# Optimization experiments

Hardware: AMD Instinct MI355X
Metric: run time of the kernel (lower is better)

The kernel has to match this reference:

```python
import jax, jax.numpy as jnp
import numpy as np

NEG = -1e4      # BigBird additive mask value
LN_EPS = 1e-12  # BERT-style LayerNorm eps


def _bigbird_forward(xs_pad, mask, Wq, bq, Wk, bk, Wv, bv, Wo, bo, gamma, beta, rand_idx):
    b, n, hsz = xs_pad.shape
    H = rand_idx.shape[0]
    nb = rand_idx.shape[1] + 2          # one rand row per non-edge query block
    BS = n // nb                        # block size
    d = hsz // H
    r = rand_idx.shape[2]
    scale = 1.0 / np.sqrt(d).astype(np.float32)

    mf = mask.reshape(b, n).astype(xs_pad.dtype)   # (b,n) 1=token, 0=pad
    mb = mf.reshape(b, nb, BS)                     # blocked mask

    def proj(W, bias):
        return (xs_pad @ W + bias).reshape(b, n, H, d).transpose(0, 2, 1, 3)

    q = proj(Wq, bq) * scale            # (b,H,n,d)
    k = proj(Wk, bk)
    v = proj(Wv, bv)
    qb = q.reshape(b, H, nb, BS, d)
    kb = k.reshape(b, H, nb, BS, d)
    vb = v.reshape(b, H, nb, BS, d)

    # ---- global rows: first / last query block attend to all keys ----
    def full_row(qi):                   # qi: (b,H,BS,d)
        s = jnp.einsum('bhqd,bhkd->bhqk', qi, k) + (1.0 - mf)[:, None, None, :] * NEG
        return jnp.einsum('bhqk,bhkd->bhqd', jax.nn.softmax(s, axis=-1), v)

    ctx_first = full_row(qb[:, :, 0])
    ctx_last = full_row(qb[:, :, nb - 1])

    # ---- random key/value blocks: per-head, per-query-block gather ----
    hidx = jnp.arange(H)[:, None, None]
    rand_k = kb[:, hidx, rand_idx].reshape(b, H, nb - 2, r * BS, d)
    rand_v = vb[:, hidx, rand_idx].reshape(b, H, nb - 2, r * BS, d)
    rand_m = mb[:, rand_idx].reshape(b, H, nb - 2, r * BS)

    def sparse_row(qi, kc, vc, mc):     # kc:(b,H,K,d), mc:(b,H,K)
        s = jnp.einsum('bhqd,bhkd->bhqk', qi, kc) + (1.0 - mc)[:, :, None, :] * NEG
        return jnp.einsum('bhqk,bhkd->bhqd', jax.nn.softmax(s, axis=-1), vc)

    def gather_blocks(ids, ridx):
        kc = jnp.concatenate([kb[:, :, j] for j in ids] + [rand_k[:, :, ridx]], axis=2)
        vc = jnp.concatenate([vb[:, :, j] for j in ids] + [rand_v[:, :, ridx]], axis=2)
        mc = jnp.concatenate([jnp.broadcast_to(mb[:, None, j], (b, H, BS)) for j in ids]
                             + [rand_m[:, :, ridx]], axis=2)
        return kc, vc, mc

    # second / penultimate query blocks: window + globals + rand
    ctx_second = sparse_row(qb[:, :, 1], *gather_blocks([0, 1, 2, nb - 1], 0))
    ctx_penult = sparse_row(qb[:, :, nb - 2], *gather_blocks([nb - 3, nb - 2, nb - 1, 0], nb - 3))

    # ---- middle rows i in [2, nb-3]: 3-block sliding window + first/last global + r random ----
    nmid = nb - 4
    mid = jnp.arange(2, nb - 2)
    win = mid[:, None] + jnp.arange(-1, 2)[None, :]        # (nmid,3)
    k_win = kb[:, :, win].reshape(b, H, nmid, 3 * BS, d)
    v_win = vb[:, :, win].reshape(b, H, nmid, 3 * BS, d)
    m_win = jnp.broadcast_to(mb[:, win].reshape(b, 1, nmid, 3 * BS), (b, H, nmid, 3 * BS))

    def rep_glob(t):                     # (b,H,BS,...) -> (b,H,nmid,BS,...)
        return jnp.broadcast_to(t[:, :, None], (b, H, nmid) + t.shape[2:])

    k_mid = jnp.concatenate([k_win, rep_glob(kb[:, :, 0]), rep_glob(kb[:, :, nb - 1]),
                             rand_k[:, :, 1:nb - 3]], axis=3)
    v_mid = jnp.concatenate([v_win, rep_glob(vb[:, :, 0]), rep_glob(vb[:, :, nb - 1]),
                             rand_v[:, :, 1:nb - 3]], axis=3)
    m_first = jnp.broadcast_to(mb[:, None, None, 0], (b, H, nmid, BS))
    m_last = jnp.broadcast_to(mb[:, None, None, nb - 1], (b, H, nmid, BS))
    m_mid = jnp.concatenate([m_win, m_first, m_last, rand_m[:, :, 1:nb - 3]], axis=3)

    s_mid = jnp.einsum('bhmqd,bhmkd->bhmqk', qb[:, :, 2:nb - 2], k_mid) \
            + (1.0 - m_mid)[:, :, :, None, :] * NEG
    ctx_mid = jnp.einsum('bhmqk,bhmkd->bhmqd', jax.nn.softmax(s_mid, axis=-1), v_mid)

    ctx = jnp.concatenate([ctx_first[:, :, None], ctx_second[:, :, None], ctx_mid,
                           ctx_penult[:, :, None], ctx_last[:, :, None]], axis=2)
    ctx = ctx.reshape(b, H, n, d).transpose(0, 2, 1, 3).reshape(b, n, hsz)
    ctx = ctx * mf[:, :, None]           # from_mask on output rows

    # BigBirdSelfOutput: dense + residual + LayerNorm (dropout=0 / eval)
    y = ctx @ Wo + bo + xs_pad
    mu = y.mean(-1, keepdims=True)
    var = ((y - mu) ** 2).mean(-1, keepdims=True)
    return (y - mu) * jax.lax.rsqrt(var + LN_EPS) * gamma + beta


def setup_inputs() -> dict:
    key = jax.random.key(0)
    ks = jax.random.split(key, 6)
    B, N, HSZ, H, BS, R = 4, 4096, 1024, 16, 64, 3
    NB = N // BS
    init = lambda k, shp: jax.random.normal(k, shp, dtype=jnp.float32) * 0.02
    return {
        'xs_pad': jax.random.normal(ks[0], (B, N, HSZ), dtype=jnp.float32),
        'mask': jnp.ones((B, 1, N), dtype=jnp.int32),
        'Wq': init(ks[1], (HSZ, HSZ)), 'bq': jnp.zeros((HSZ,), jnp.float32),
        'Wk': init(ks[2], (HSZ, HSZ)), 'bk': jnp.zeros((HSZ,), jnp.float32),
        'Wv': init(ks[3], (HSZ, HSZ)), 'bv': jnp.zeros((HSZ,), jnp.float32),
        'Wo': init(ks[4], (HSZ, HSZ)), 'bo': jnp.zeros((HSZ,), jnp.float32),
        'gamma': jnp.ones((HSZ,), jnp.float32), 'beta': jnp.zeros((HSZ,), jnp.float32),
        'rand_idx': jax.random.randint(ks[5], (H, NB - 2, R), 1, NB - 1).astype(jnp.int32),
    }


def reference(xs_pad, mask, Wq, bq, Wk, bk, Wv, bv, Wo, bo, gamma, beta, rand_idx):
    return _bigbird_forward(xs_pad, mask, Wq, bq, Wk, bk, Wv, bv, Wo, bo, gamma, beta, rand_idx)
```

## Files before the change

### kernel.cpp

```cpp
#include <hip/hip_runtime.h>
#include <hip/hip_bf16.h>

#define B_   4
#define N_   4096
#define HSZ  1024
#define H_   16
#define D_   64
#define NB_  64
#define R_   3
#define M_   (B_*N_)
#define NEGV (-1e4f)
#define LOG2E 1.4426950408889634f

typedef float f32x4 __attribute__((ext_vector_type(4)));
typedef short s16x8 __attribute__((ext_vector_type(8)));
typedef __bf16 b16x8 __attribute__((ext_vector_type(8)));

__device__ __forceinline__ f32x4 mfma16(s16x8 a, s16x8 b, f32x4 c) {
  return __builtin_amdgcn_mfma_f32_16x16x32_bf16(
      __builtin_bit_cast(b16x8, a), __builtin_bit_cast(b16x8, b), c, 0, 0, 0);
}

__device__ __forceinline__ short f2b(float x) {
  __hip_bfloat16 h = __float2bfloat16(x);
  return (short)__builtin_bit_cast(unsigned short, h);
}

__device__ __forceinline__ unsigned pack2(float a, float b) {
  return (unsigned)(unsigned short)f2b(a) |
         ((unsigned)(unsigned short)f2b(b) << 16);
}

__device__ __forceinline__ void gl_lds16(const short* g, short* l) {
  __builtin_amdgcn_global_load_lds(
      (const __attribute__((address_space(1))) unsigned int*)g,
      (__attribute__((address_space(3))) unsigned int*)l, 16, 0, 0);
}

__global__ __launch_bounds__(256) void k_conv(const float* __restrict__ in,
                                              short* __restrict__ out) {
  size_t i = ((size_t)blockIdx.x * 256 + threadIdx.x) * 8;
  float4 a = *(const float4*)&in[i];
  float4 b = *(const float4*)&in[i + 4];
  s16x8 o;
  o[0] = f2b(a.x); o[1] = f2b(a.y); o[2] = f2b(a.z); o[3] = f2b(a.w);
  o[4] = f2b(b.x); o[5] = f2b(b.y); o[6] = f2b(b.z); o[7] = f2b(b.w);
  *(s16x8*)&out[i] = o;
}

__global__ __launch_bounds__(256) void k_wt(const float* __restrict__ Wq,
                                            const float* __restrict__ Wk,
                                            const float* __restrict__ Wv,
                                            const float* __restrict__ Wo,
                                            short* __restrict__ out) {
  const int z = blockIdx.z;
  const float* src = (z == 0) ? Wq : (z == 1) ? Wk : (z == 2) ? Wv : Wo;
  short* dst = out + (size_t)z * HSZ * HSZ;
  __shared__ __align__(16) float t[64][68];
  const int tk = blockIdx.x * 64, tn = blockIdx.y * 64;
  const int tid = threadIdx.x;
#pragma unroll
  for (int r = 0; r < 4; ++r) {
    int c = tid + r * 256;
    int row = c >> 4, seg = c & 15;
    *(float4*)&t[row][seg * 4] =
        *(const float4*)&src[(size_t)(tk + row) * HSZ + tn + seg * 4];
  }
  __syncthreads();
#pragma unroll
  for (int r = 0; r < 2; ++r) {
    int c = tid + r * 256;
    int row = c >> 3, seg = c & 7;
    s16x8 o;
#pragma unroll
    for (int u = 0; u < 8; ++u) o[u] = f2b(t[seg * 8 + u][row]);
    *(s16x8*)&dst[(size_t)(tn + row) * HSZ + tk + seg * 8] = o;
  }
}

template <int PATH>
__global__ __launch_bounds__(256) void k_gemm(
    const short* __restrict__ A, const short* __restrict__ WT,
    const float* __restrict__ bias0, const float* __restrict__ bias1,
    short* __restrict__ o0, short* __restrict__ o1,
    const float* __restrict__ xs, float* __restrict__ yout) {
  const int z = (PATH == 0) ? blockIdx.z : 0;
  const int wsel = (PATH == 0) ? z : (PATH == 1 ? 2 : 3);
  const short* Bt = WT + (size_t)wsel * HSZ * HSZ;
  const float* bias = (PATH == 0 && z == 1) ? bias1 : bias0;
  short* outb = (PATH == 0 && z == 1) ? o1 : o0;
  const float alpha = (PATH == 0 && z == 0) ? 0.125f * LOG2E : 1.0f;

  __shared__ __align__(16) short a_lds[2][128][64];
  __shared__ __align__(16) short b_lds[2][128][64];

  const int tid = threadIdx.x, lane = tid & 63, wave = tid >> 6;
  const int lq = lane & 15, g = lane >> 4;
  const int wm = (wave & 1) * 64, wn = (wave >> 1) * 64;
  const int tm = blockIdx.x * 128, tn = blockIdx.y * 128;

  const int srow = wave * 32 + (lane >> 3);
  const int scol = ((lane & 7) ^ ((lane >> 3) & 7)) * 8;

  f32x4 acc[4][4] = {};

  auto STAGE = [&](int buf, int kt) {
#pragma unroll
    for (int u = 0; u < 4; ++u) {
      gl_lds16(&A[(size_t)(tm + srow + u * 8) * HSZ + kt + scol],
               &a_lds[buf][wave * 32 + u * 8][0]);
      gl_lds16(&Bt[(size_t)(tn + srow + u * 8) * HSZ + kt + scol],
               &b_lds[buf][wave * 32 + u * 8][0]);
    }
  };

  const int sw = (lq & 7) << 3;
  auto COMPUTE = [&](int buf) {
#pragma unroll
    for (int kk = 0; kk < 2; ++kk) {
      const int ko = (kk * 32 + g * 8) ^ sw;
      s16x8 af[4], bf[4];
#pragma unroll
      for (int i = 0; i < 4; ++i)
        af[i] = *(const s16x8*)&a_lds[buf][wm + i * 16 + lq][ko];
#pragma unroll
      for (int j = 0; j < 4; ++j)
        bf[j] = *(const s16x8*)&b_lds[buf][wn + j * 16 + lq][ko];
#pragma unroll
      for (int i = 0; i < 4; ++i)
#pragma unroll
        for (int j = 0; j < 4; ++j)
          acc[i][j] = (PATH == 1) ? mfma16(af[i], bf[j], acc[i][j])
                                  : mfma16(bf[j], af[i], acc[i][j]);
    }
  };

  STAGE(0, 0);
  STAGE(1, 64);
  int cur = 0;
  for (int s = 0; s < 14; ++s) {
    asm volatile("s_waitcnt vmcnt(8)" ::: "memory");
    __builtin_amdgcn_s_barrier();
    COMPUTE(cur);
    __builtin_amdgcn_s_barrier();
    STAGE(cur, (s + 2) * 64);
    cur ^= 1;
  }
  asm volatile("s_waitcnt vmcnt(8)" ::: "memory");
  __builtin_amdgcn_s_barrier();
  COMPUTE(cur);
  cur ^= 1;
  asm volatile("s_waitcnt vmcnt(0)" ::: "memory");
  __builtin_amdgcn_s_barrier();
  COMPUTE(cur);

  if (PATH == 1) {
#pragma unroll
    for (int j = 0; j < 4; ++j) {
      const int col = tn + wn + j * 16 + lq;
      const int hh = col >> 6, dd = col & 63;
      const float bi = bias[col];
#pragma unroll
      for (int i = 0; i < 4; ++i) {
        const int nrow = tm + wm + i * 16 + g * 4;
        const int bb = nrow >> 12, nn = nrow & (N_ - 1);
        uint2 w;
        w.x = pack2(acc[i][j][0] + bi, acc[i][j][1] + bi);
        w.y = pack2(acc[i][j][2] + bi, acc[i][j][3] + bi);
        *(uint2*)&o0[(((size_t)bb * H_ + hh) * D_ + dd) * N_ + nn] = w;
      }
    }
    return;
  }

#pragma unroll
  for (int i = 0; i < 4; ++i) {
    const int row = tm + wm + i * 16 + lq;
#pragma unroll
    for (int j = 0; j < 4; ++j) {
      const int colb = tn + wn + j * 16 + g * 4;
      const float4 bi = *(const float4*)&bias[colb];
      if (PATH == 0) {
        const int bb = row >> 12, nn = row & (N_ - 1);
        const int hh = colb >> 6, dd = colb & 63;
        uint2 w;
        w.x = pack2((acc[i][j][0] + bi.x) * alpha,
                    (acc[i][j][1] + bi.y) * alpha);
        w.y = pack2((acc[i][j][2] + bi.z) * alpha,
                    (acc[i][j][3] + bi.w) * alpha);
        *(uint2*)&outb[(((size_t)bb * H_ + hh) * N_ + nn) * D_ + dd] = w;
      } else {
        const size_t idx = (size_t)row * HSZ + colb;
        const float4 xv = *(const float4*)&xs[idx];
        float4 yv;
        yv.x = acc[i][j][0] + bi.x + xv.x;
        yv.y = acc[i][j][1] + bi.y + xv.y;
        yv.z = acc[i][j][2] + bi.z + xv.z;
        yv.w = acc[i][j][3] + bi.w + xv.w;
        *(float4*)&yout[idx] = yv;
      }
    }
  }
}

__global__ __launch_bounds__(256) void k_attn(
    const short* __restrict__ Q, const short* __restrict__ K,
    const short* __restrict__ VT, const int* __restrict__ mask,
    const int* __restrict__ rnd, short* __restrict__ ctx,
    float* __restrict__ pO, float* __restrict__ pm, float* __restrict__ pl) {
  const int s = blockIdx.x, h = blockIdx.y, b = blockIdx.z;
  const int tid = threadIdx.x, lane = tid & 63, wave = tid >> 6;
  const int g = lane >> 4, lq = lane & 15;

  __shared__ __align__(16) short k_lds[64][72];
  __shared__ __align__(16) short vt_lds[64][72];
  __shared__ __align__(16) short p_lds[4][16][72];
  __shared__ __align__(16) float bias_s[64];
  __shared__ int list_s[8];
  __shared__ int Ls;

  const bool mid = (s < 62);
  const int qb = mid ? (s + 1) : (((s - 62) >> 3) ? (NB_ - 1) : 0);

  if (tid == 0) {
    int L;
    if (!mid) {
      int chunk = (s - 62) & 7;
#pragma unroll
      for (int i = 0; i < 8; ++i) list_s[i] = chunk * 8 + i;
      L = 8;
    } else {
      const int* rp = rnd + ((size_t)h * (NB_ - 2) + (qb - 1)) * R_;
      int n;
      if (qb == 1) {
        list_s[0] = 0; list_s[1] = 1; list_s[2] = 2; list_s[3] = NB_ - 1; n = 4;
      } else if (qb == NB_ - 2) {
        list_s[0] = NB_ - 3; list_s[1] = NB_ - 2; list_s[2] = NB_ - 1;
        list_s[3] = 0; n = 4;
      } else {
        list_s[0] = qb - 1; list_s[1] = qb; list_s[2] = qb + 1;
        list_s[3] = 0; list_s[4] = NB_ - 1; n = 5;
      }
      for (int j = 0; j < R_; ++j) list_s[n + j] = rp[j];
      L = n + R_;
    }
    Ls = L;
  }

  const size_t bh = (size_t)b * H_ + h;
  const size_t qrow = bh * N_ + (size_t)qb * 64 + wave * 16 + lq;
  s16x8 qf0 = *(const s16x8*)&Q[qrow * D_ + g * 8];
  s16x8 qf1 = *(const s16x8*)&Q[qrow * D_ + 32 + g * 8];

  __syncthreads();
  const int L = Ls;

  const int r0 = tid >> 3, sg0 = tid & 7;
  const int r1 = 32 + (tid >> 3), sg1 = tid & 7;

  s16x8 kr0, kr1, vr0, vr1;
  float br = 0.0f;
  {
    const int kb = list_s[0];
    const short* kp = &K[(bh * N_ + (size_t)kb * 64) * D_];
    const short* vp = &VT[bh * (size_t)D_ * N_ + (size_t)kb * 64];
    kr0 = *(const s16x8*)&kp[r0 * D_ + sg0 * 8];
    kr1 = *(const s16x8*)&kp[r1 * D_ + sg1 * 8];
    vr0 = *(const s16x8*)&vp[(size_t)r0 * N_ + sg0 * 8];
    vr1 = *(const s16x8*)&vp[(size_t)r1 * N_ + sg1 * 8];
    if (tid < 64)
      br = (1.0f - (float)mask[(size_t)b * N_ + kb * 64 + tid]) *
           (NEGV * LOG2E);
  }

  f32x4 o[4] = {};
  float m_run = -INFINITY, ssum = 0.0f;

  for (int it = 0; it < L; ++it) {
    *(s16x8*)&k_lds[r0][sg0 * 8] = kr0;
    *(s16x8*)&k_lds[r1][sg1 * 8] = kr1;
    *(s16x8*)&vt_lds[r0][sg0 * 8] = vr0;
    *(s16x8*)&vt_lds[r1][sg1 * 8] = vr1;
    if (tid < 64) bias_s[tid] = br;
    if (it + 1 < L) {
      const int kb = list_s[it + 1];
      const short* kp = &K[(bh * N_ + (size_t)kb * 64) * D_];
      const short* vp = &VT[bh * (size_t)D_ * N_ + (size_t)kb * 64];
      kr0 = *(const s16x8*)&kp[r0 * D_ + sg0 * 8];
      kr1 = *(const s16x8*)&kp[r1 * D_ + sg1 * 8];
      vr0 = *(const s16x8*)&vp[(size_t)r0 * N_ + sg0 * 8];
      vr1 = *(const s16x8*)&vp[(size_t)r1 * N_ + sg1 * 8];
      if (tid < 64)
        br = (1.0f - (float)mask[(size_t)b * N_ + kb * 64 + tid]) *
             (NEGV * LOG2E);
    }
    __syncthreads();

    f32x4 st[4];
#pragma unroll
    for (int f = 0; f < 4; ++f) {
      f32x4 acc0 = {};
#pragma unroll
      for (int kk = 0; kk < 2; ++kk) {
        s16x8 af = *(const s16x8*)&k_lds[f * 16 + lq][kk * 32 + g * 8];
        acc0 = mfma16(af, kk ? qf1 : qf0, acc0);
      }
      f32x4 b4 = *(const f32x4*)&bias_s[f * 16 + g * 4];
      st[f] = acc0 + b4;
    }

    float t0 = fmaxf(fmaxf(st[0][0], st[0][1]), fmaxf(st[0][2], st[0][3]));
    float t1 = fmaxf(fmaxf(st[1][0], st[1][1]), fmaxf(st[1][2], st[1][3]));
    float t2 = fmaxf(fmaxf(st[2][0], st[2][1]), fmaxf(st[2][2], st[2][3]));
    float t3 = fmaxf(fmaxf(st[3][0], st[3][1]), fmaxf(st[3][2], st[3][3]));
    float bm = fmaxf(fmaxf(t0, t1), fmaxf(t2, t3));
    bm = fmaxf(bm, __shfl_xor(bm, 16));
    bm = fmaxf(bm, __shfl_xor(bm, 32));
    if (!__all(bm <= m_run + 8.0f)) {
      float mnew = fmaxf(m_run, bm);
      float al = exp2f(m_run - mnew);
      f32x4 av;
      av[0] = __shfl(al, g * 4 + 0);
      av[1] = __shfl(al, g * 4 + 1);
      av[2] = __shfl(al, g * 4 + 2);
      av[3] = __shfl(al, g * 4 + 3);
#pragma unroll
      for (int j = 0; j < 4; ++j) o[j] *= av;
      ssum *= al;
      m_run = mnew;
    }
    float psum = 0.0f;
#pragma unroll
    for (int f = 0; f < 4; ++f)
#pragma unroll
      for (int e = 0; e < 4; ++e) {
        float p = exp2f(st[f][e] - m_run);
        st[f][e] = p;
        psum += p;
      }
    psum += __shfl_xor(psum, 16);
    psum += __shfl_xor(psum, 32);
    ssum += psum;

#pragma unroll
    for (int f = 0; f < 4; ++f) {
      uint2 w = make_uint2(pack2(st[f][0], st[f][1]),
                           pack2(st[f][2], st[f][3]));
      *(uint2*)&p_lds[wave][lq][f * 16 + g * 4] = w;
    }

#pragma unroll
    for (int kk = 0; kk < 2; ++kk) {
      s16x8 pa = *(const s16x8*)&p_lds[wave][lq][kk * 32 + g * 8];
#pragma unroll
      for (int j = 0; j < 4; ++j) {
        s16x8 bv = *(const s16x8*)&vt_lds[j * 16 + lq][kk * 32 + g * 8];
        o[j] = mfma16(pa, bv, o[j]);
      }
    }
    __syncthreads();
  }

  if (mid) {
    float rs = (float)mask[(size_t)b * N_ + qb * 64 + wave * 16 + lq] / ssum;
    float s0 = __shfl(rs, g * 4 + 0);
    float s1 = __shfl(rs, g * 4 + 1);
    float s2 = __shfl(rs, g * 4 + 2);
    float s3 = __shfl(rs, g * 4 + 3);
#pragma unroll
    for (int j = 0; j < 4; ++j) {
      k_lds[wave * 16 + g * 4 + 0][j * 16 + lq] = f2b(o[j][0] * s0);
      k_lds[wave * 16 + g * 4 + 1][j * 16 + lq] = f2b(o[j][1] * s1);
      k_lds[wave * 16 + g * 4 + 2][j * 16 + lq] = f2b(o[j][2] * s2);
      k_lds[wave * 16 + g * 4 + 3][j * 16 + lq] = f2b(o[j][3] * s3);
    }
    __syncthreads();
#pragma unroll
    for (int p = 0; p < 2; ++p) {
      int c = tid + p * 256;
      int row = c >> 3, seg = c & 7;
      *(s16x8*)&ctx[((size_t)b * N_ + qb * 64 + row) * HSZ + h * D_ + seg * 8] =
          *(const s16x8*)&k_lds[row][seg * 8];
    }
  } else {
    const int e2 = s - 62;
    const int qsel = e2 >> 3, chunk = e2 & 7;
    const size_t eidx = (bh * 2 + qsel) * 8 + chunk;
    float* po = pO + eidx * 4096;
#pragma unroll
    for (int j = 0; j < 4; ++j)
#pragma unroll
      for (int e = 0; e < 4; ++e)
        po[(wave * 16 + g * 4 + e) * 64 + j * 16 + lq] = o[j][e];
    if (lane < 16) {
      pm[eidx * 64 + wave * 16 + lane] = m_run;
      pl[eidx * 64 + wave * 16 + lane] = ssum;
    }
  }
}

__global__ __launch_bounds__(256) void k_comb(
    const float* __restrict__ pO, const float* __restrict__ pm,
    const float* __restrict__ pl, const int* __restrict__ mask,
    short* __restrict__ ctx) {
  const int qsel = blockIdx.x, h = blockIdx.y, b = blockIdx.z;
  const int qb = qsel ? NB_ - 1 : 0;
  const int tid = threadIdx.x;
  const int q = tid >> 2, dq = tid & 3;
  const size_t base = (((size_t)b * H_ + h) * 2 + qsel) * 8;

  float mv[8];
  float M = -INFINITY;
#pragma unroll
  for (int i = 0; i < 8; ++i) {
    mv[i] = pm[(base + i) * 64 + q];
    M = fmaxf(M, mv[i]);
  }
  float Lsum = 0.0f;
#pragma unroll
  for (int i = 0; i < 8; ++i) {
    float w = exp2f(mv[i] - M);
    mv[i] = w;
    Lsum += pl[(base + i) * 64 + q] * w;
  }
  f32x4 acc[4] = {};
#pragma unroll
  for (int i = 0; i < 8; ++i) {
    const float* p = pO + (base + i) * 4096 + q * 64 + dq * 16;
    float w = mv[i];
#pragma unroll
    for (int u = 0; u < 4; ++u) {
      f32x4 v = *(const f32x4*)&p[u * 4];
      acc[u] += v * w;
    }
  }
  float sc = (float)mask[(size_t)b * N_ + qb * 64 + q] / Lsum;
  s16x8 out0, out1;
#pragma unroll
  for (int u = 0; u < 8; ++u) {
    out0[u] = f2b(acc[u >> 2][u & 3] * sc);
    out1[u] = f2b(acc[2 + (u >> 2)][u & 3] * sc);
  }
  short* dst = &ctx[((size_t)b * N_ + qb * 64 + q) * HSZ + h * D_ + dq * 16];
  *(s16x8*)dst = out0;
  *(s16x8*)(dst + 8) = out1;
}

__global__ __launch_bounds__(256) void k_ln(float* __restrict__ y,
                                            const float* __restrict__ gamma,
                                            const float* __restrict__ beta) {
  const int row = blockIdx.x, tid = threadIdx.x, lane = tid & 63,
            wave = tid >> 6;
  __shared__ float s_sum[4], s_sq[4];
  float4 v = *(const float4*)&y[(size_t)row * HSZ + tid * 4];
  float s = v.x + v.y + v.z + v.w;
  float q = v.x * v.x + v.y * v.y + v.z * v.z + v.w * v.w;
#pragma unroll
  for (int m = 1; m <= 32; m <<= 1) {
    s += __shfl_xor(s, m);
    q += __shfl_xor(q, m);
  }
  if (lane == 0) { s_sum[wave] = s; s_sq[wave] = q; }
  __syncthreads();
  float S = s_sum[0] + s_sum[1] + s_sum[2] + s_sum[3];
  float Qs = s_sq[0] + s_sq[1] + s_sq[2] + s_sq[3];
  float mu = S * (1.0f / HSZ);
  float var = Qs * (1.0f / HSZ) - mu * mu;
  float r = rsqrtf(var + 1e-12f);
  float4 g = *(const float4*)&gamma[tid * 4];
  float4 be = *(const float4*)&beta[tid * 4];
  float4 outv;
  outv.x = (v.x - mu) * r * g.x + be.x;
  outv.y = (v.y - mu) * r * g.y + be.y;
  outv.z = (v.z - mu) * r * g.z + be.z;
  outv.w = (v.w - mu) * r * g.w + be.w;
  *(float4*)&y[(size_t)row * HSZ + tid * 4] = outv;
}

extern "C" void kernel_launch(void* const* d_in, const int* in_sizes, int n_in,
                              void* d_out, int out_size, void* d_ws,
                              size_t ws_size, hipStream_t stream) {
  const float* xs = (const float*)d_in[0];
  const int* mask = (const int*)d_in[1];
  const float* Wq = (const float*)d_in[2];
  const float* bq = (const float*)d_in[3];
  const float* Wk = (const float*)d_in[4];
  const float* bk = (const float*)d_in[5];
  const float* Wv = (const float*)d_in[6];
  const float* bv = (const float*)d_in[7];
  const float* Wo = (const float*)d_in[8];
  const float* bo = (const float*)d_in[9];
  const float* gamma = (const float*)d_in[10];
  const float* beta = (const float*)d_in[11];
  const int* rnd = (const int*)d_in[12];
  float* yout = (float*)d_out;

  char* ws = (char*)d_ws;
  const size_t SZ_XS = (size_t)M_ * HSZ * 2;
  const size_t SZ_WT = (size_t)4 * HSZ * HSZ * 2;
  short* xsb = (short*)ws;
  short* wt = (short*)(ws + SZ_XS);
  short* qbuf = (short*)(ws + SZ_XS + SZ_WT);
  short* kbuf = qbuf + (size_t)M_ * HSZ;
  short* vtb = kbuf + (size_t)M_ * HSZ;
  char* after = ws + SZ_XS + SZ_WT + 3 * SZ_XS;
  float* pO = (float*)(after + (1 << 20));
  float* pm = pO + (size_t)1024 * 4096;
  float* pl = pm + (size_t)1024 * 64;

  k_conv<<<8192, 256, 0, stream>>>(xs, xsb);
  k_wt<<<dim3(16, 16, 4), 256, 0, stream>>>(Wq, Wk, Wv, Wo, wt);
  k_gemm<0><<<dim3(128, 8, 2), 256, 0, stream>>>(
      xsb, wt, bq, bk, qbuf, kbuf, nullptr, nullptr);
  k_gemm<1><<<dim3(128, 8, 1), 256, 0, stream>>>(
      xsb, wt, bv, nullptr, vtb, nullptr, nullptr, nullptr);
  k_attn<<<dim3(78, H_, B_), 256, 0, stream>>>(qbuf, kbuf, vtb, mask, rnd,
                                               xsb, pO, pm, pl);
  k_comb<<<dim3(2, H_, B_), 256, 0, stream>>>(pO, pm, pl, mask, xsb);
  k_gemm<2><<<dim3(128, 8, 1), 256, 0, stream>>>(
      xsb, wt, bo, nullptr, nullptr, nullptr, xs, yout);
  k_ln<<<M_, 256, 0, stream>>>(yout, gamma, beta);
}
```

Baseline: 365.7 us.

## Process key blocks in pairs with swizzled LDS and XCD-aware block remap

The attention kernel now loads two 64-key blocks per iteration, so an iteration works on 128 keys. This halves the number of barriers and online-softmax rescale steps, and an odd block list is padded with a fully masked dummy block. The LDS tiles drop their row padding in favour of an XOR swizzle to avoid bank conflicts. The 3D grid is flattened and remapped so that consecutive workgroups of the same head/batch spread across XCDs. The trade-off is more registers and LDS per block and some wasted work on the padded blocks.

```diff
diff --git a/kernel.cpp b/kernel.cpp
--- a/kernel.cpp
+++ b/kernel.cpp
@@ -208,14 +208,18 @@
     const short* __restrict__ VT, const int* __restrict__ mask,
     const int* __restrict__ rnd, short* __restrict__ ctx,
     float* __restrict__ pO, float* __restrict__ pm, float* __restrict__ pl) {
-  const int s = blockIdx.x, h = blockIdx.y, b = blockIdx.z;
+  const int orig = blockIdx.x;
+  const int swg = (orig & 7) * 624 + (orig >> 3);
+  const int s = swg % 78;
+  const int bh_i = swg / 78;
+  const int h = bh_i & 15, b = bh_i >> 4;
   const int tid = threadIdx.x, lane = tid & 63, wave = tid >> 6;
   const int g = lane >> 4, lq = lane & 15;
 
-  __shared__ __align__(16) short k_lds[64][72];
-  __shared__ __align__(16) short vt_lds[64][72];
-  __shared__ __align__(16) short p_lds[4][16][72];
-  __shared__ __align__(16) float bias_s[64];
+  __shared__ __align__(16) short k_lds[128][64];
+  __shared__ __align__(16) short vt_lds[64][128];
+  __shared__ __align__(16) short p_lds[4][16][136];
+  __shared__ __align__(16) float bias_s[128];
   __shared__ int list_s[8];
   __shared__ int Ls;
 
@@ -243,6 +247,7 @@
       }
       for (int j = 0; j < R_; ++j) list_s[n + j] = rp[j];
       L = n + R_;
+      if (L & 1) list_s[L] = 0;
     }
     Ls = L;
   }
@@ -254,66 +259,73 @@
 
   __syncthreads();
   const int L = Ls;
-
-  const int r0 = tid >> 3, sg0 = tid & 7;
-  const int r1 = 32 + (tid >> 3), sg1 = tid & 7;
-
-  s16x8 kr0, kr1, vr0, vr1;
-  float br = 0.0f;
-  {
-    const int kb = list_s[0];
-    const short* kp = &K[(bh * N_ + (size_t)kb * 64) * D_];
-    const short* vp = &VT[bh * (size_t)D_ * N_ + (size_t)kb * 64];
-    kr0 = *(const s16x8*)&kp[r0 * D_ + sg0 * 8];
-    kr1 = *(const s16x8*)&kp[r1 * D_ + sg1 * 8];
-    vr0 = *(const s16x8*)&vp[(size_t)r0 * N_ + sg0 * 8];
-    vr1 = *(const s16x8*)&vp[(size_t)r1 * N_ + sg1 * 8];
-    if (tid < 64)
-      br = (1.0f - (float)mask[(size_t)b * N_ + kb * 64 + tid]) *
-           (NEGV * LOG2E);
-  }
+  const int npairs = (L + 1) >> 1;
+
+  const int r0 = tid >> 3, sg = tid & 7;
+  const int csl = (sg ^ (r0 & 7)) * 8;
+
+  const short* Kb = K + bh * (size_t)N_ * D_;
+  const short* Vb = VT + bh * (size_t)D_ * N_;
+  const int* mb = mask + (size_t)b * N_;
+
+  s16x8 krA0, krA1, krB0, krB1, vrA0, vrA1, vrB0, vrB1;
+  float brv = 0.0f;
+
+  auto LOADP = [&](int p) {
+    const int kA = list_s[2 * p], kB = list_s[2 * p + 1];
+    const bool padB = (2 * p + 1 >= L);
+    const short* kpA = Kb + (size_t)kA * 64 * D_;
+    const short* kpB = Kb + (size_t)kB * 64 * D_;
+    const short* vpA = Vb + (size_t)kA * 64;
+    const short* vpB = Vb + (size_t)kB * 64;
+    krA0 = *(const s16x8*)&kpA[(size_t)r0 * D_ + sg * 8];
+    krA1 = *(const s16x8*)&kpA[(size_t)(r0 + 32) * D_ + sg * 8];
+    krB0 = *(const s16x8*)&kpB[(size_t)r0 * D_ + sg * 8];
+    krB1 = *(const s16x8*)&kpB[(size_t)(r0 + 32) * D_ + sg * 8];
+    vrA0 = *(const s16x8*)&vpA[(size_t)r0 * N_ + sg * 8];
+    vrA1 = *(const s16x8*)&vpA[(size_t)(r0 + 32) * N_ + sg * 8];
+    vrB0 = *(const s16x8*)&vpB[(size_t)r0 * N_ + sg * 8];
+    vrB1 = *(const s16x8*)&vpB[(size_t)(r0 + 32) * N_ + sg * 8];
+    if (tid < 128) {
+      const int kb = (tid < 64) ? kA : kB;
+      const float m = (float)mb[kb * 64 + (tid & 63)];
+      brv = (padB && tid >= 64) ? -1.0e5f : (1.0f - m) * (NEGV * LOG2E);
+    }
+  };
 
   f32x4 o[4] = {};
   float m_run = -INFINITY, ssum = 0.0f;
 
-  for (int it = 0; it < L; ++it) {
-    *(s16x8*)&k_lds[r0][sg0 * 8] = kr0;
-    *(s16x8*)&k_lds[r1][sg1 * 8] = kr1;
-    *(s16x8*)&vt_lds[r0][sg0 * 8] = vr0;
-    *(s16x8*)&vt_lds[r1][sg1 * 8] = vr1;
-    if (tid < 64) bias_s[tid] = br;
-    if (it + 1 < L) {
-      const int kb = list_s[it + 1];
-      const short* kp = &K[(bh * N_ + (size_t)kb * 64) * D_];
-      const short* vp = &VT[bh * (size_t)D_ * N_ + (size_t)kb * 64];
-      kr0 = *(const s16x8*)&kp[r0 * D_ + sg0 * 8];
-      kr1 = *(const s16x8*)&kp[r1 * D_ + sg1 * 8];
-      vr0 = *(const s16x8*)&vp[(size_t)r0 * N_ + sg0 * 8];
-      vr1 = *(const s16x8*)&vp[(size_t)r1 * N_ + sg1 * 8];
-      if (tid < 64)
-        br = (1.0f - (float)mask[(size_t)b * N_ + kb * 64 + tid]) *
-             (NEGV * LOG2E);
-    }
+  LOADP(0);
+  for (int p = 0; p < npairs; ++p) {
+    *(s16x8*)&k_lds[r0][csl] = krA0;
+    *(s16x8*)&k_lds[r0 + 32][csl] = krA1;
+    *(s16x8*)&k_lds[r0 + 64][csl] = krB0;
+    *(s16x8*)&k_lds[r0 + 96][csl] = krB1;
+    *(s16x8*)&vt_lds[r0][csl] = vrA0;
+    *(s16x8*)&vt_lds[r0 + 32][csl] = vrA1;
+    *(s16x8*)&vt_lds[r0][64 + csl] = vrB0;
+    *(s16x8*)&vt_lds[r0 + 32][64 + csl] = vrB1;
+    if (tid < 128) bias_s[tid] = brv;
+    if (p + 1 < npairs) LOADP(p + 1);
     __syncthreads();
 
-    f32x4 st[4];
-#pragma unroll
-    for (int f = 0; f < 4; ++f) {
-      f32x4 acc0 = {};
-#pragma unroll
-      for (int kk = 0; kk < 2; ++kk) {
-        s16x8 af = *(const s16x8*)&k_lds[f * 16 + lq][kk * 32 + g * 8];
-        acc0 = mfma16(af, kk ? qf1 : qf0, acc0);
-      }
-      f32x4 b4 = *(const f32x4*)&bias_s[f * 16 + g * 4];
-      st[f] = acc0 + b4;
-    }
-
-    float t0 = fmaxf(fmaxf(st[0][0], st[0][1]), fmaxf(st[0][2], st[0][3]));
-    float t1 = fmaxf(fmaxf(st[1][0], st[1][1]), fmaxf(st[1][2], st[1][3]));
-    float t2 = fmaxf(fmaxf(st[2][0], st[2][1]), fmaxf(st[2][2], st[2][3]));
-    float t3 = fmaxf(fmaxf(st[3][0], st[3][1]), fmaxf(st[3][2], st[3][3]));
-    float bm = fmaxf(fmaxf(t0, t1), fmaxf(t2, t3));
+    f32x4 st[8];
+#pragma unroll
+    for (int f = 0; f < 8; ++f) {
+      f32x4 a0 = {};
+      s16x8 af0 = *(const s16x8*)&k_lds[f * 16 + lq][(g ^ (lq & 7)) * 8];
+      s16x8 af1 = *(const s16x8*)&k_lds[f * 16 + lq][((4 + g) ^ (lq & 7)) * 8];
+      a0 = mfma16(af0, qf0, a0);
+      a0 = mfma16(af1, qf1, a0);
+      st[f] = a0 + *(const f32x4*)&bias_s[f * 16 + g * 4];
+    }
+
+    float bm = -INFINITY;
+#pragma unroll
+    for (int f = 0; f < 8; ++f)
+#pragma unroll
+      for (int e = 0; e < 4; ++e) bm = fmaxf(bm, st[f][e]);
     bm = fmaxf(bm, __shfl_xor(bm, 16));
     bm = fmaxf(bm, __shfl_xor(bm, 32));
     if (!__all(bm <= m_run + 8.0f)) {
@@ -331,30 +343,32 @@
     }
     float psum = 0.0f;
 #pragma unroll
-    for (int f = 0; f < 4; ++f)
+    for (int f = 0; f < 8; ++f)
 #pragma unroll
       for (int e = 0; e < 4; ++e) {
-        float p = exp2f(st[f][e] - m_run);
-        st[f][e] = p;
-        psum += p;
+        float pv = exp2f(st[f][e] - m_run);
+        st[f][e] = pv;
+        psum += pv;
       }
     psum += __shfl_xor(psum, 16);
     psum += __shfl_xor(psum, 32);
     ssum += psum;
 
 #pragma unroll
-    for (int f = 0; f < 4; ++f) {
+    for (int f = 0; f < 8; ++f) {
       uint2 w = make_uint2(pack2(st[f][0], st[f][1]),
                            pack2(st[f][2], st[f][3]));
       *(uint2*)&p_lds[wave][lq][f * 16 + g * 4] = w;
     }
 
 #pragma unroll
-    for (int kk = 0; kk < 2; ++kk) {
+    for (int kk = 0; kk < 4; ++kk) {
       s16x8 pa = *(const s16x8*)&p_lds[wave][lq][kk * 32 + g * 8];
+      const int slot = kk * 4 + g;
+      const int col = ((slot & 8) | ((slot ^ lq) & 7)) * 8;
 #pragma unroll
       for (int j = 0; j < 4; ++j) {
-        s16x8 bv = *(const s16x8*)&vt_lds[j * 16 + lq][kk * 32 + g * 8];
+        s16x8 bv = *(const s16x8*)&vt_lds[j * 16 + lq][col];
         o[j] = mfma16(pa, bv, o[j]);
       }
     }
@@ -362,25 +376,26 @@
   }
 
   if (mid) {
-    float rs = (float)mask[(size_t)b * N_ + qb * 64 + wave * 16 + lq] / ssum;
+    float rs = (float)mb[qb * 64 + wave * 16 + lq] / ssum;
     float s0 = __shfl(rs, g * 4 + 0);
     float s1 = __shfl(rs, g * 4 + 1);
     float s2 = __shfl(rs, g * 4 + 2);
     float s3 = __shfl(rs, g * 4 + 3);
+    short (*ost)[136] = reinterpret_cast<short(*)[136]>(&p_lds[0][0][0]);
 #pragma unroll
     for (int j = 0; j < 4; ++j) {
-      k_lds[wave * 16 + g * 4 + 0][j * 16 + lq] = f2b(o[j][0] * s0);
-      k_lds[wave * 16 + g * 4 + 1][j * 16 + lq] = f2b(o[j][1] * s1);
-      k_lds[wave * 16 + g * 4 + 2][j * 16 + lq] = f2b(o[j][2] * s2);
-      k_lds[wave * 16 + g * 4 + 3][j * 16 + lq] = f2b(o[j][3] * s3);
+      ost[wave * 16 + g * 4 + 0][j * 16 + lq] = f2b(o[j][0] * s0);
+      ost[wave * 16 + g * 4 + 1][j * 16 + lq] = f2b(o[j][1] * s1);
+      ost[wave * 16 + g * 4 + 2][j * 16 + lq] = f2b(o[j][2] * s2);
+      ost[wave * 16 + g * 4 + 3][j * 16 + lq] = f2b(o[j][3] * s3);
     }
     __syncthreads();
 #pragma unroll
-    for (int p = 0; p < 2; ++p) {
-      int c = tid + p * 256;
+    for (int pp = 0; pp < 2; ++pp) {
+      int c = tid + pp * 256;
       int row = c >> 3, seg = c & 7;
       *(s16x8*)&ctx[((size_t)b * N_ + qb * 64 + row) * HSZ + h * D_ + seg * 8] =
-          *(const s16x8*)&k_lds[row][seg * 8];
+          *(const s16x8*)&ost[row][seg * 8];
     }
   } else {
     const int e2 = s - 62;
@@ -514,8 +529,8 @@
       xsb, wt, bq, bk, qbuf, kbuf, nullptr, nullptr);
   k_gemm<1><<<dim3(128, 8, 1), 256, 0, stream>>>(
       xsb, wt, bv, nullptr, vtb, nullptr, nullptr, nullptr);
-  k_attn<<<dim3(78, H_, B_), 256, 0, stream>>>(qbuf, kbuf, vtb, mask, rnd,
-                                               xsb, pO, pm, pl);
+  k_attn<<<4992, 256, 0, stream>>>(qbuf, kbuf, vtb, mask, rnd, xsb, pO, pm,
+                                   pl);
   k_comb<<<dim3(2, H_, B_), 256, 0, stream>>>(pO, pm, pl, mask, xsb);
   k_gemm<2><<<dim3(128, 8, 1), 256, 0, stream>>>(
       xsb, wt, bo, nullptr, nullptr, nullptr, xs, yout);
```

Measured after the change: 381.3 us. 4.3% more time.
